# Performance work log

Hardware: AMD Instinct MI355X
Metric: run time of the kernel (lower is better)

## Reference

```python
import jax, jax.numpy as jnp
import numpy as np

B, C, H, W = 4, 256, 64, 64
CQK = C // 8  # query/key channel dim per the module (out_channels // 8)
EPS = 1e-5    # BatchNorm eps


def _make_proj(key, c_out, c_in):
    kw, km = jax.random.split(key)
    w = jax.random.normal(kw, (c_out, c_in), jnp.float32) * (1.0 / np.sqrt(c_in))
    b = jnp.zeros((c_out,), jnp.float32)
    bn_g = jnp.ones((c_out,), jnp.float32)
    bn_b = jnp.zeros((c_out,), jnp.float32)
    bn_mean = jax.random.normal(km, (c_out,), jnp.float32) * 0.1
    bn_var = jnp.ones((c_out,), jnp.float32) * 0.9  # positive running var
    return w, b, bn_g, bn_b, bn_mean, bn_var


def setup_inputs() -> dict:
    key = jax.random.key(0)
    kx, kq, kk, kv = jax.random.split(key, 4)
    x = jax.random.normal(kx, (B, C, H, W), jnp.float32)
    q_w, q_b, q_g, q_beta, q_mean, q_var = _make_proj(kq, CQK, C)
    k_w, k_b, k_g, k_beta, k_mean, k_var = _make_proj(kk, CQK, C)
    v_w, v_b, v_g, v_beta, v_mean, v_var = _make_proj(kv, C, C)
    gamma = jnp.array([0.5], jnp.float32)  # nn.Parameter(zeros(1)); nonzero to exercise attention path
    return dict(x=x,
                q_w=q_w, q_b=q_b, q_g=q_g, q_beta=q_beta, q_mean=q_mean, q_var=q_var,
                k_w=k_w, k_b=k_b, k_g=k_g, k_beta=k_beta, k_mean=k_mean, k_var=k_var,
                v_w=v_w, v_b=v_b, v_g=v_g, v_beta=v_beta, v_mean=v_mean, v_var=v_var,
                gamma=gamma)


def _conv1x1_bn(xf, w, b, g, beta, mean, var):
    # xf: [B, Cin, N]; 1x1 conv == channel matmul, BN in eval mode (running stats)
    y = jnp.einsum('oc,bcn->bon', w, xf) + b[None, :, None]
    scale = (g * jax.lax.rsqrt(var + EPS))[None, :, None]
    shift = (beta - mean * g * jax.lax.rsqrt(var + EPS))[None, :, None]
    return y * scale + shift


def reference(x,
              q_w, q_b, q_g, q_beta, q_mean, q_var,
              k_w, k_b, k_g, k_beta, k_mean, k_var,
              v_w, v_b, v_g, v_beta, v_mean, v_var,
              gamma):
    b_, c_, h_, w_ = x.shape
    n = h_ * w_
    xf = x.reshape(b_, c_, n)  # z = x (z is None path)
    q = _conv1x1_bn(xf, q_w, q_b, q_g, q_beta, q_mean, q_var)  # [B, C/8, N]
    k = _conv1x1_bn(xf, k_w, k_b, k_g, k_beta, k_mean, k_var)  # [B, C/8, N]
    v = _conv1x1_bn(xf, v_w, v_b, v_g, v_beta, v_mean, v_var)  # [B, C,   N]
    # attention[b, i, j] = softmax_j(q[b,:,i] . k[b,:,j])
    attn = jax.nn.softmax(jnp.einsum('bci,bcj->bij', q, k), axis=-1)
    # out[b, c, i] = sum_j v[b, c, j] * attn[b, i, j]
    out = jnp.einsum('bcj,bij->bci', v, attn).reshape(b_, c_, h_, w_)
    return gamma[0] * out + x
```

## Files before the change

kernel.cpp:

```cpp
#include <hip/hip_runtime.h>
#include <hip/hip_bf16.h>

#define B_     4
#define C_     256
#define CQK_   32
#define N_     4096
#define NSTK_  320
#define EPS_   1e-5f
#define JSPLIT 4
#define JCHUNK (N_ / JSPLIT)
#define NSTEP  (JCHUNK / 64)
#define L2E_   1.4426950408889634f

typedef short  bf16x8  __attribute__((ext_vector_type(8)));
typedef float  f32x4   __attribute__((ext_vector_type(4)));
typedef float  f32x16  __attribute__((ext_vector_type(16)));
typedef unsigned short u16x4 __attribute__((ext_vector_type(4)));

union PAU { unsigned u[4]; bf16x8 v; };

__device__ __forceinline__ unsigned pk_bf16(float lo, float hi) {
  __hip_bfloat16 ha = __float2bfloat16(lo);
  __hip_bfloat16 hb = __float2bfloat16(hi);
  unsigned short ua = *reinterpret_cast<unsigned short*>(&ha);
  unsigned short ub = *reinterpret_cast<unsigned short*>(&hb);
  return (unsigned)ua | ((unsigned)ub << 16);
}
__device__ __forceinline__ void pl32swap(unsigned &a, unsigned &b) {
  asm("v_permlane32_swap_b32 %0, %1" : "+v"(a), "+v"(b));
}

__global__ __launch_bounds__(256) void prep_w_kernel(
    const float* qw, const float* qb, const float* qg, const float* qbe, const float* qm, const float* qv,
    const float* kw, const float* kb, const float* kg, const float* kbe, const float* km, const float* kv,
    const float* vw, const float* vb, const float* vg, const float* vbe, const float* vm, const float* vv,
    __hip_bfloat16* Wp, float* bias)
{
  int idx = blockIdx.x * 256 + threadIdx.x;
  const int total = NSTK_ * C_;
  if (idx < total) {
    int o = idx >> 8, c = idx & 255;
    const float *w, *g, *var; int oo; float mul = 1.f;
    if (o < 32)      { w = qw; g = qg; var = qv; oo = o;      mul = L2E_; }
    else if (o < 64) { w = kw; g = kg; var = kv; oo = o - 32; }
    else             { w = vw; g = vg; var = vv; oo = o - 64; }
    float sc = g[oo] * rsqrtf(var[oo] + EPS_) * mul;
    Wp[idx] = __float2bfloat16(w[oo * C_ + c] * sc);
  } else if (idx < total + NSTK_) {
    int o = idx - total;
    const float *bb, *g, *var, *be, *mn; int oo; float mul = 1.f;
    if (o < 32)      { bb = qb; g = qg; var = qv; be = qbe; mn = qm; oo = o;      mul = L2E_; }
    else if (o < 64) { bb = kb; g = kg; var = kv; be = kbe; mn = km; oo = o - 32; }
    else             { bb = vb; g = vg; var = vv; be = vbe; mn = vm; oo = o - 64; }
    float sc = g[oo] * rsqrtf(var[oo] + EPS_);
    bias[o] = (bb[oo] * sc + be[oo] - mn[oo] * sc) * mul;
  }
}

__global__ __launch_bounds__(256, 4) void proj_kernel(
    const __hip_bfloat16* __restrict__ Wp, const float* __restrict__ bias,
    const float* __restrict__ x,
    __hip_bfloat16* __restrict__ QT, __hip_bfloat16* __restrict__ KT,
    __hip_bfloat16* __restrict__ V)
{
  __shared__ __align__(16) __hip_bfloat16 tile[32 * 264];

  int b = blockIdx.y, n0 = blockIdx.x * 32;
  int t = threadIdx.x, w = t >> 6, l = t & 63;
  int l15 = l & 15, kg8 = (l >> 4) * 8;

  {
    int ln = t & 31, cg = t >> 5;
    #pragma unroll 8
    for (int it = 0; it < 32; ++it) {
      int c = it * 8 + cg;
      float v = x[((size_t)b * C_ + c) * N_ + n0 + ln];
      tile[ln * 264 + c] = __float2bfloat16(v);
    }
  }
  __syncthreads();

  const int o0 = w * 80;
  f32x4 acc[5][2];
  #pragma unroll
  for (int ot = 0; ot < 5; ++ot)
    #pragma unroll
    for (int nt = 0; nt < 2; ++nt) acc[ot][nt] = (f32x4){0.f, 0.f, 0.f, 0.f};

  for (int k0 = 0; k0 < C_; k0 += 32) {
    bf16x8 bb[2];
    #pragma unroll
    for (int nt = 0; nt < 2; ++nt)
      bb[nt] = *(const bf16x8*)(tile + (nt * 16 + l15) * 264 + k0 + kg8);
    #pragma unroll
    for (int ot = 0; ot < 5; ++ot) {
      bf16x8 a = *(const bf16x8*)(Wp + (size_t)(o0 + ot * 16 + l15) * C_ + k0 + kg8);
      acc[ot][0] = __builtin_amdgcn_mfma_f32_16x16x32_bf16(a, bb[0], acc[ot][0], 0, 0, 0);
      acc[ot][1] = __builtin_amdgcn_mfma_f32_16x16x32_bf16(a, bb[1], acc[ot][1], 0, 0, 0);
    }
  }

  int rbase = (l >> 4) * 4;
  #pragma unroll
  for (int ot = 0; ot < 5; ++ot) {
    #pragma unroll
    for (int nt = 0; nt < 2; ++nt) {
      #pragma unroll
      for (int r = 0; r < 4; ++r) {
        int o = o0 + ot * 16 + rbase + r;
        int n = n0 + nt * 16 + l15;
        __hip_bfloat16 hv = __float2bfloat16(acc[ot][nt][r] + bias[o]);
        if (o < 32)        QT[((size_t)b * N_ + n) * CQK_ + o]        = hv;
        else if (o < 64)   KT[((size_t)b * N_ + n) * CQK_ + (o - 32)] = hv;
        else               V[((size_t)b * C_ + (o - 64)) * N_ + n]    = hv;
      }
    }
  }
}

__device__ __forceinline__ void stage_v(const __hip_bfloat16* __restrict__ Vg,
                                        const __hip_bfloat16* dstbase,
                                        int bc_base, int j0, int tid)
{
  #pragma unroll
  for (int q = 0; q < 4; ++q) {
    const int c = q * 64 + (tid >> 3);
    const int s = tid & 7;
    const int jb = ((s ^ (c & 7)) << 3);
    const __hip_bfloat16* src = Vg + ((size_t)(bc_base + c)) * N_ + j0 + jb;
    const __hip_bfloat16* dst = dstbase + (size_t)(q * 512 + tid) * 8;
    __builtin_amdgcn_global_load_lds((const __attribute__((address_space(1))) void*)src,
                                     (__attribute__((address_space(3))) void*)dst, 16, 0, 0);
  }
}

__global__ __launch_bounds__(512, 1) void attn_kernel(
    const __hip_bfloat16* __restrict__ QT, const __hip_bfloat16* __restrict__ KT,
    const __hip_bfloat16* __restrict__ V,
    __hip_bfloat16* __restrict__ Opart, float* __restrict__ lstat)
{
  __shared__ __align__(16) __hip_bfloat16 vtile[2][256 * 64];

  const int b = blockIdx.z;
  const int jcid = blockIdx.y;
  const int i0 = blockIdx.x * 256;
  const int t = threadIdx.x;
  const int w = t >> 6, l = t & 63;
  const int l31 = l & 31, hi = l >> 5;
  const int ibase = i0 + w * 32;
  const int jbase = jcid * JCHUNK;
  const int c7 = l31 & 7;

  bf16x8 qf[2];
  #pragma unroll
  for (int kc = 0; kc < 2; ++kc)
    qf[kc] = *(const bf16x8*)(QT + ((size_t)b * N_ + ibase + l31) * CQK_ + kc * 16 + hi * 8);

  f32x16 oacc[8];
  #pragma unroll
  for (int ct = 0; ct < 8; ++ct)
    #pragma unroll
    for (int r = 0; r < 16; ++r) oacc[ct][r] = 0.f;

  float l_run = 0.f;

  bf16x8 kf[2][2];
  #pragma unroll
  for (int jt = 0; jt < 2; ++jt)
    #pragma unroll
    for (int kc = 0; kc < 2; ++kc)
      kf[jt][kc] = *(const bf16x8*)(KT + ((size_t)b * N_ + jbase + jt * 32 + l31) * CQK_ + kc * 16 + hi * 8);
  stage_v(V, vtile[0], b * C_, jbase, t);
  __syncthreads();

  for (int st = 0; st < NSTEP; ++st) {
    const int j0 = jbase + st * 64;
    const __hip_bfloat16* vb = vtile[st & 1];
    const bool more = (st + 1 < NSTEP);

    if (more) stage_v(V, vtile[(st + 1) & 1], b * C_, j0 + 64, t);

    f32x16 s0, s1;
    #pragma unroll
    for (int r = 0; r < 16; ++r) { s0[r] = 0.f; s1[r] = 0.f; }
    #pragma unroll
    for (int kc = 0; kc < 2; ++kc) {
      s0 = __builtin_amdgcn_mfma_f32_32x32x16_bf16(kf[0][kc], qf[kc], s0, 0, 0, 0);
      s1 = __builtin_amdgcn_mfma_f32_32x32x16_bf16(kf[1][kc], qf[kc], s1, 0, 0, 0);
    }

    bf16x8 kfn[2][2];
    if (more) {
      #pragma unroll
      for (int jt = 0; jt < 2; ++jt)
        #pragma unroll
        for (int kc = 0; kc < 2; ++kc)
          kfn[jt][kc] = *(const bf16x8*)(KT + ((size_t)b * N_ + j0 + 64 + jt * 32 + l31) * CQK_ + kc * 16 + hi * 8);
    }

    float p0[16], p1[16];
    #pragma unroll
    for (int r = 0; r < 16; ++r) {
      p0[r] = __builtin_amdgcn_exp2f(s0[r]);
      p1[r] = __builtin_amdgcn_exp2f(s1[r]);
    }
    {
      float t0 = 0.f, t1 = 0.f, t2 = 0.f, t3 = 0.f;
      #pragma unroll
      for (int r = 0; r < 16; r += 4) {
        t0 += p0[r] + p1[r];     t1 += p0[r + 1] + p1[r + 1];
        t2 += p0[r + 2] + p1[r + 2]; t3 += p0[r + 3] + p1[r + 3];
      }
      l_run += (t0 + t1) + (t2 + t3);
    }
    bf16x8 pa[4];
    {
      unsigned u0 = pk_bf16(p0[0], p0[1]),  u1 = pk_bf16(p0[2], p0[3]);
      unsigned u2 = pk_bf16(p0[4], p0[5]),  u3 = pk_bf16(p0[6], p0[7]);
      pl32swap(u0, u2); pl32swap(u1, u3);
      PAU pu; pu.u[0] = u0; pu.u[1] = u1; pu.u[2] = u2; pu.u[3] = u3;
      pa[0] = pu.v;
      u0 = pk_bf16(p0[8],  p0[9]);  u1 = pk_bf16(p0[10], p0[11]);
      u2 = pk_bf16(p0[12], p0[13]); u3 = pk_bf16(p0[14], p0[15]);
      pl32swap(u0, u2); pl32swap(u1, u3);
      pu.u[0] = u0; pu.u[1] = u1; pu.u[2] = u2; pu.u[3] = u3;
      pa[1] = pu.v;
      u0 = pk_bf16(p1[0], p1[1]);  u1 = pk_bf16(p1[2], p1[3]);
      u2 = pk_bf16(p1[4], p1[5]);  u3 = pk_bf16(p1[6], p1[7]);
      pl32swap(u0, u2); pl32swap(u1, u3);
      pu.u[0] = u0; pu.u[1] = u1; pu.u[2] = u2; pu.u[3] = u3;
      pa[2] = pu.v;
      u0 = pk_bf16(p1[8],  p1[9]);  u1 = pk_bf16(p1[10], p1[11]);
      u2 = pk_bf16(p1[12], p1[13]); u3 = pk_bf16(p1[14], p1[15]);
      pl32swap(u0, u2); pl32swap(u1, u3);
      pu.u[0] = u0; pu.u[1] = u1; pu.u[2] = u2; pu.u[3] = u3;
      pa[3] = pu.v;
    }

    #pragma unroll
    for (int jc = 0; jc < 4; ++jc) {
      const int joff = (((jc << 1) + hi) ^ c7) << 3;
      __builtin_amdgcn_s_setprio(1);
      #pragma unroll
      for (int ct = 0; ct < 8; ++ct) {
        const int c = ct * 32 + l31;
        bf16x8 va = *(const bf16x8*)(vb + c * 64 + joff);
        oacc[ct] = __builtin_amdgcn_mfma_f32_32x32x16_bf16(va, pa[jc], oacc[ct], 0, 0, 0);
      }
      __builtin_amdgcn_s_setprio(0);
    }

    __syncthreads();

    if (more) {
      #pragma unroll
      for (int jt = 0; jt < 2; ++jt)
        #pragma unroll
        for (int kc = 0; kc < 2; ++kc)
          kf[jt][kc] = kfn[jt][kc];
    }
  }

  {
    float lt = l_run + __shfl_xor(l_run, 32);
    const int irow = ibase + l31;
    if (hi == 0) {
      size_t sidx = ((size_t)jcid * B_ + b) * N_ + irow;
      lstat[sidx] = lt;
    }
    #pragma unroll
    for (int ct = 0; ct < 8; ++ct) {
      #pragma unroll
      for (int q = 0; q < 4; ++q) {
        const int c = ct * 32 + 4 * hi + 8 * q;
        __hip_bfloat16* dst = Opart + (((size_t)jcid * B_ + b) * C_ + c) * N_ + irow;
        dst[0]              = __float2bfloat16(oacc[ct][q * 4 + 0]);
        dst[N_]             = __float2bfloat16(oacc[ct][q * 4 + 1]);
        dst[2 * (size_t)N_] = __float2bfloat16(oacc[ct][q * 4 + 2]);
        dst[3 * (size_t)N_] = __float2bfloat16(oacc[ct][q * 4 + 3]);
      }
    }
  }
}

__global__ __launch_bounds__(256) void combine_kernel(
    const __hip_bfloat16* __restrict__ Opart, const float* __restrict__ lstat,
    const float* __restrict__ x, const float* __restrict__ gamma,
    float* __restrict__ out)
{
  const int b = blockIdx.z, cg = blockIdx.y;
  const int i4 = blockIdx.x * 1024 + threadIdx.x * 4;
  const float gm = gamma[0];

  f32x4 L = (f32x4){0.f, 0.f, 0.f, 0.f};
  #pragma unroll
  for (int p = 0; p < JSPLIT; ++p)
    L += *(const f32x4*)(lstat + ((size_t)p * B_ + b) * N_ + i4);
  f32x4 sc;
  #pragma unroll
  for (int e = 0; e < 4; ++e) sc[e] = gm / L[e];

  #pragma unroll
  for (int cc = 0; cc < 8; ++cc) {
    const int c = cg * 8 + cc;
    const size_t rb = ((size_t)b * C_ + c) * N_ + i4;
    f32x4 acc = (f32x4){0.f, 0.f, 0.f, 0.f};
    #pragma unroll
    for (int p = 0; p < JSPLIT; ++p) {
      u16x4 ov = *(const u16x4*)(Opart + (((size_t)p * B_ + b) * C_ + c) * N_ + i4);
      #pragma unroll
      for (int e = 0; e < 4; ++e) {
        unsigned ubits = ((unsigned)ov[e]) << 16;
        acc[e] += *reinterpret_cast<float*>(&ubits);
      }
    }
    f32x4 z = *(const f32x4*)(x + rb);
    #pragma unroll
    for (int e = 0; e < 4; ++e) z[e] += sc[e] * acc[e];
    *(f32x4*)(out + rb) = z;
  }
}

extern "C" void kernel_launch(void* const* d_in, const int* in_sizes, int n_in,
                              void* d_out, int out_size, void* d_ws, size_t ws_size,
                              hipStream_t stream)
{
  const float* x   = (const float*)d_in[0];
  const float* qw  = (const float*)d_in[1];
  const float* qb  = (const float*)d_in[2];
  const float* qg  = (const float*)d_in[3];
  const float* qbe = (const float*)d_in[4];
  const float* qm  = (const float*)d_in[5];
  const float* qv  = (const float*)d_in[6];
  const float* kw  = (const float*)d_in[7];
  const float* kb  = (const float*)d_in[8];
  const float* kg  = (const float*)d_in[9];
  const float* kbe = (const float*)d_in[10];
  const float* km  = (const float*)d_in[11];
  const float* kv  = (const float*)d_in[12];
  const float* vw  = (const float*)d_in[13];
  const float* vb  = (const float*)d_in[14];
  const float* vg  = (const float*)d_in[15];
  const float* vbe = (const float*)d_in[16];
  const float* vm  = (const float*)d_in[17];
  const float* vv  = (const float*)d_in[18];
  const float* gamma = (const float*)d_in[19];

  char* ws = (char*)d_ws;
  __hip_bfloat16* Wp  = (__hip_bfloat16*)(ws + 0);
  float*          bias = (float*)        (ws + 163840);
  __hip_bfloat16* QT  = (__hip_bfloat16*)(ws + 165376);
  __hip_bfloat16* KT  = (__hip_bfloat16*)(ws + 1213952);
  __hip_bfloat16* V   = (__hip_bfloat16*)(ws + 2262528);
  __hip_bfloat16* Opart = (__hip_bfloat16*)(ws + 10651136);
  float* lstat = (float*)(ws + 44205568);
  float* out = (float*)d_out;

  prep_w_kernel<<<(NSTK_ * C_ + NSTK_ + 255) / 256, 256, 0, stream>>>(
      qw, qb, qg, qbe, qm, qv, kw, kb, kg, kbe, km, kv, vw, vb, vg, vbe, vm, vv, Wp, bias);
  proj_kernel<<<dim3(N_ / 32, B_), 256, 0, stream>>>(Wp, bias, x, QT, KT, V);
  attn_kernel<<<dim3(N_ / 256, JSPLIT, B_), 512, 0, stream>>>(QT, KT, V, Opart, lstat);
  combine_kernel<<<dim3(N_ / 1024, C_ / 8, B_), 256, 0, stream>>>(Opart, lstat, x, gamma, out);
}
```

Before: 80.68 us.

## Split attention block waves across key halves and reduce partials through LDS

Each attention block now covers 128 query rows instead of 256. Its eight waves form four query groups times two key halves, so each wave computes one 32-wide S tile per step instead of two and runs half the PV MFMAs. The grid doubles to 512 blocks, which should fill more CUs and shorten per-block latency. The cost is twice as many blocks staging the same V tiles, plus an end-of-kernel reduction through LDS in which one wave half writes bf16 partials that the other adds before storing. That intermediate bf16 rounding of the partial sums adds some precision loss.

Measured after the change: 93.16 us. 15.5% more time.

```diff
diff --git a/kernel.cpp b/kernel.cpp
--- a/kernel.cpp
+++ b/kernel.cpp
@@ -28,6 +28,10 @@
 }
 __device__ __forceinline__ void pl32swap(unsigned &a, unsigned &b) {
   asm("v_permlane32_swap_b32 %0, %1" : "+v"(a), "+v"(b));
+}
+__device__ __forceinline__ float bf2f(unsigned short u) {
+  unsigned ub = ((unsigned)u) << 16;
+  return *reinterpret_cast<float*>(&ub);
 }
 
 __global__ __launch_bounds__(256) void prep_w_kernel(
@@ -140,15 +144,18 @@
     __hip_bfloat16* __restrict__ Opart, float* __restrict__ lstat)
 {
   __shared__ __align__(16) __hip_bfloat16 vtile[2][256 * 64];
+  __shared__ float lxch[4][32];
 
   const int b = blockIdx.z;
   const int jcid = blockIdx.y;
-  const int i0 = blockIdx.x * 256;
+  const int i0 = blockIdx.x * 128;
   const int t = threadIdx.x;
   const int w = t >> 6, l = t & 63;
   const int l31 = l & 31, hi = l >> 5;
-  const int ibase = i0 + w * 32;
+  const int si = w & 3, jh = w >> 2;
+  const int ibase = i0 + si * 32;
   const int jbase = jcid * JCHUNK;
+  const int jwav = jh * 32;
   const int c7 = l31 & 7;
 
   bf16x8 qf[2];
@@ -164,12 +171,10 @@
 
   float l_run = 0.f;
 
-  bf16x8 kf[2][2];
-  #pragma unroll
-  for (int jt = 0; jt < 2; ++jt)
-    #pragma unroll
-    for (int kc = 0; kc < 2; ++kc)
-      kf[jt][kc] = *(const bf16x8*)(KT + ((size_t)b * N_ + jbase + jt * 32 + l31) * CQK_ + kc * 16 + hi * 8);
+  bf16x8 kf[2];
+  #pragma unroll
+  for (int kc = 0; kc < 2; ++kc)
+    kf[kc] = *(const bf16x8*)(KT + ((size_t)b * N_ + jbase + jwav + l31) * CQK_ + kc * 16 + hi * 8);
   stage_v(V, vtile[0], b * C_, jbase, t);
   __syncthreads();
 
@@ -180,66 +185,47 @@
 
     if (more) stage_v(V, vtile[(st + 1) & 1], b * C_, j0 + 64, t);
 
-    f32x16 s0, s1;
-    #pragma unroll
-    for (int r = 0; r < 16; ++r) { s0[r] = 0.f; s1[r] = 0.f; }
-    #pragma unroll
-    for (int kc = 0; kc < 2; ++kc) {
-      s0 = __builtin_amdgcn_mfma_f32_32x32x16_bf16(kf[0][kc], qf[kc], s0, 0, 0, 0);
-      s1 = __builtin_amdgcn_mfma_f32_32x32x16_bf16(kf[1][kc], qf[kc], s1, 0, 0, 0);
-    }
-
-    bf16x8 kfn[2][2];
+    f32x16 s;
+    #pragma unroll
+    for (int r = 0; r < 16; ++r) s[r] = 0.f;
+    #pragma unroll
+    for (int kc = 0; kc < 2; ++kc)
+      s = __builtin_amdgcn_mfma_f32_32x32x16_bf16(kf[kc], qf[kc], s, 0, 0, 0);
+
+    bf16x8 kfn[2];
     if (more) {
       #pragma unroll
-      for (int jt = 0; jt < 2; ++jt)
-        #pragma unroll
-        for (int kc = 0; kc < 2; ++kc)
-          kfn[jt][kc] = *(const bf16x8*)(KT + ((size_t)b * N_ + j0 + 64 + jt * 32 + l31) * CQK_ + kc * 16 + hi * 8);
-    }
-
-    float p0[16], p1[16];
-    #pragma unroll
-    for (int r = 0; r < 16; ++r) {
-      p0[r] = __builtin_amdgcn_exp2f(s0[r]);
-      p1[r] = __builtin_amdgcn_exp2f(s1[r]);
-    }
+      for (int kc = 0; kc < 2; ++kc)
+        kfn[kc] = *(const bf16x8*)(KT + ((size_t)b * N_ + j0 + 64 + jwav + l31) * CQK_ + kc * 16 + hi * 8);
+    }
+
+    float p[16];
+    #pragma unroll
+    for (int r = 0; r < 16; ++r) p[r] = __builtin_amdgcn_exp2f(s[r]);
     {
-      float t0 = 0.f, t1 = 0.f, t2 = 0.f, t3 = 0.f;
-      #pragma unroll
-      for (int r = 0; r < 16; r += 4) {
-        t0 += p0[r] + p1[r];     t1 += p0[r + 1] + p1[r + 1];
-        t2 += p0[r + 2] + p1[r + 2]; t3 += p0[r + 3] + p1[r + 3];
-      }
+      float t0 = p[0] + p[4] + p[8]  + p[12];
+      float t1 = p[1] + p[5] + p[9]  + p[13];
+      float t2 = p[2] + p[6] + p[10] + p[14];
+      float t3 = p[3] + p[7] + p[11] + p[15];
       l_run += (t0 + t1) + (t2 + t3);
     }
-    bf16x8 pa[4];
+    bf16x8 pa[2];
     {
-      unsigned u0 = pk_bf16(p0[0], p0[1]),  u1 = pk_bf16(p0[2], p0[3]);
-      unsigned u2 = pk_bf16(p0[4], p0[5]),  u3 = pk_bf16(p0[6], p0[7]);
+      unsigned u0 = pk_bf16(p[0], p[1]),  u1 = pk_bf16(p[2], p[3]);
+      unsigned u2 = pk_bf16(p[4], p[5]),  u3 = pk_bf16(p[6], p[7]);
       pl32swap(u0, u2); pl32swap(u1, u3);
       PAU pu; pu.u[0] = u0; pu.u[1] = u1; pu.u[2] = u2; pu.u[3] = u3;
       pa[0] = pu.v;
-      u0 = pk_bf16(p0[8],  p0[9]);  u1 = pk_bf16(p0[10], p0[11]);
-      u2 = pk_bf16(p0[12], p0[13]); u3 = pk_bf16(p0[14], p0[15]);
+      u0 = pk_bf16(p[8],  p[9]);  u1 = pk_bf16(p[10], p[11]);
+      u2 = pk_bf16(p[12], p[13]); u3 = pk_bf16(p[14], p[15]);
       pl32swap(u0, u2); pl32swap(u1, u3);
       pu.u[0] = u0; pu.u[1] = u1; pu.u[2] = u2; pu.u[3] = u3;
       pa[1] = pu.v;
-      u0 = pk_bf16(p1[0], p1[1]);  u1 = pk_bf16(p1[2], p1[3]);
-      u2 = pk_bf16(p1[4], p1[5]);  u3 = pk_bf16(p1[6], p1[7]);
-      pl32swap(u0, u2); pl32swap(u1, u3);
-      pu.u[0] = u0; pu.u[1] = u1; pu.u[2] = u2; pu.u[3] = u3;
-      pa[2] = pu.v;
-      u0 = pk_bf16(p1[8],  p1[9]);  u1 = pk_bf16(p1[10], p1[11]);
-      u2 = pk_bf16(p1[12], p1[13]); u3 = pk_bf16(p1[14], p1[15]);
-      pl32swap(u0, u2); pl32swap(u1, u3);
-      pu.u[0] = u0; pu.u[1] = u1; pu.u[2] = u2; pu.u[3] = u3;
-      pa[3] = pu.v;
-    }
-
-    #pragma unroll
-    for (int jc = 0; jc < 4; ++jc) {
-      const int joff = (((jc << 1) + hi) ^ c7) << 3;
+    }
+
+    #pragma unroll
+    for (int jc = 0; jc < 2; ++jc) {
+      const int joff = (((jh << 2) + (jc << 1) + hi) ^ c7) << 3;
       __builtin_amdgcn_s_setprio(1);
       #pragma unroll
       for (int ct = 0; ct < 8; ++ct) {
@@ -253,31 +239,46 @@
     __syncthreads();
 
     if (more) {
-      #pragma unroll
-      for (int jt = 0; jt < 2; ++jt)
+      kf[0] = kfn[0]; kf[1] = kfn[1];
+    }
+  }
+
+  float lt = l_run + __shfl_xor(l_run, 32);
+
+  __syncthreads();
+  __hip_bfloat16* xb = (__hip_bfloat16*)vtile;
+  if (jh == 1) {
+    #pragma unroll
+    for (int ct = 0; ct < 8; ++ct) {
+      #pragma unroll
+      for (int q = 0; q < 4; ++q) {
         #pragma unroll
-        for (int kc = 0; kc < 2; ++kc)
-          kf[jt][kc] = kfn[jt][kc];
-    }
-  }
-
-  {
-    float lt = l_run + __shfl_xor(l_run, 32);
+        for (int r = 0; r < 4; ++r) {
+          const int c = ct * 32 + 4 * hi + 8 * q + r;
+          xb[si * 8192 + c * 32 + l31] = __float2bfloat16(oacc[ct][q * 4 + r]);
+        }
+      }
+    }
+    if (hi == 0) lxch[si][l31] = lt;
+  }
+  __syncthreads();
+  if (jh == 0) {
     const int irow = ibase + l31;
     if (hi == 0) {
       size_t sidx = ((size_t)jcid * B_ + b) * N_ + irow;
-      lstat[sidx] = lt;
+      lstat[sidx] = lt + lxch[si][l31];
     }
     #pragma unroll
     for (int ct = 0; ct < 8; ++ct) {
       #pragma unroll
       for (int q = 0; q < 4; ++q) {
-        const int c = ct * 32 + 4 * hi + 8 * q;
-        __hip_bfloat16* dst = Opart + (((size_t)jcid * B_ + b) * C_ + c) * N_ + irow;
-        dst[0]              = __float2bfloat16(oacc[ct][q * 4 + 0]);
-        dst[N_]             = __float2bfloat16(oacc[ct][q * 4 + 1]);
-        dst[2 * (size_t)N_] = __float2bfloat16(oacc[ct][q * 4 + 2]);
-        dst[3 * (size_t)N_] = __float2bfloat16(oacc[ct][q * 4 + 3]);
+        #pragma unroll
+        for (int r = 0; r < 4; ++r) {
+          const int c = ct * 32 + 4 * hi + 8 * q + r;
+          unsigned short ub = *reinterpret_cast<unsigned short*>(&xb[si * 8192 + c * 32 + l31]);
+          float o = oacc[ct][q * 4 + r] + bf2f(ub);
+          Opart[(((size_t)jcid * B_ + b) * C_ + c) * N_ + irow] = __float2bfloat16(o);
+        }
       }
     }
   }
@@ -359,6 +360,6 @@
   prep_w_kernel<<<(NSTK_ * C_ + NSTK_ + 255) / 256, 256, 0, stream>>>(
       qw, qb, qg, qbe, qm, qv, kw, kb, kg, kbe, km, kv, vw, vb, vg, vbe, vm, vv, Wp, bias);
   proj_kernel<<<dim3(N_ / 32, B_), 256, 0, stream>>>(Wp, bias, x, QT, KT, V);
-  attn_kernel<<<dim3(N_ / 256, JSPLIT, B_), 512, 0, stream>>>(QT, KT, V, Opart, lstat);
+  attn_kernel<<<dim3(N_ / 128, JSPLIT, B_), 512, 0, stream>>>(QT, KT, V, Opart, lstat);
   combine_kernel<<<dim3(N_ / 1024, C_ / 8, B_), 256, 0, stream>>>(Opart, lstat, x, gamma, out);
 }
```
